# Kernel optimization log

Hardware: AMD Instinct MI355X
Metric: run time of the kernel (lower is better)

The kernel has to match this reference:

```python
import jax, jax.numpy as jnp
import numpy as np


def setup_inputs() -> dict:
    key = jax.random.key(0)
    k1, k2 = jax.random.split(key)
    B, S, D = 8, 2048, 1024
    head = jax.random.normal(k1, (B, S, D), dtype=jnp.float32)
    tail = jax.random.normal(k2, (B, S, D), dtype=jnp.float32)
    return {"head": head, "tail": tail}


def reference(head, tail):
    # head: [B, Sh, D], tail: [B, St, D]; temperature = 1/sqrt(D)
    D = tail.shape[2]
    temperature = 1.0 / jnp.sqrt(jnp.asarray(D, dtype=tail.dtype))
    # scores: [B, St, Sh] = tail @ head^T, scaled
    scores = jnp.einsum('btd,bhd->bth', tail, head) * temperature
    # softmax over the head axis (last dim)
    weight = jax.nn.softmax(scores, axis=-1)
    # pred_tails: [B, St, D] (requires Sh == St, as in the original matmul)
    pred_tails = jnp.einsum('bth,bhd->btd', weight, tail)
    return pred_tails
```

## Files before the change

### kernel.cpp

```cpp
#include <hip/hip_runtime.h>
#include <stdint.h>

typedef __attribute__((ext_vector_type(4))) float f32x4;
typedef __attribute__((ext_vector_type(4))) unsigned int u32x4;
typedef __attribute__((ext_vector_type(8))) __bf16 bf16x8;

#define NB 8
#define SQ 2048
#define DM 1024

__device__ __forceinline__ bf16x8 ldfrag(const __bf16* base, int row, int chunk) {
  const char* p = (const char*)base + row * 128 + ((chunk ^ (row & 7)) << 4);
  return *(const bf16x8*)p;
}

__global__ void k_convert(const float* __restrict__ src, __bf16* __restrict__ dst) {
  size_t i = (size_t)blockIdx.x * blockDim.x + threadIdx.x;
  const f32x4* s = (const f32x4*)src + i * 2;
  f32x4 a = s[0], b = s[1];
  bf16x8 o;
  o[0] = (__bf16)a[0]; o[1] = (__bf16)a[1]; o[2] = (__bf16)a[2]; o[3] = (__bf16)a[3];
  o[4] = (__bf16)b[0]; o[5] = (__bf16)b[1]; o[6] = (__bf16)b[2]; o[7] = (__bf16)b[3];
  *((bf16x8*)dst + i) = o;
}

__global__ void k_transpose(const float* __restrict__ V, __bf16* __restrict__ Vt) {
  __shared__ alignas(16) __bf16 sT[64 * 72];
  const int tid = threadIdx.x;
  const int d0 = blockIdx.x * 64, h0 = blockIdx.y * 64, b = blockIdx.z;
#pragma unroll
  for (int p = 0; p < 4; ++p) {
    int r = (tid >> 4) + p * 16;
    int c4 = (tid & 15) * 4;
    f32x4 v = *(const f32x4*)&V[((size_t)(b * SQ + h0 + r)) * DM + d0 + c4];
#pragma unroll
    for (int j = 0; j < 4; ++j) sT[(c4 + j) * 72 + r] = (__bf16)v[j];
  }
  __syncthreads();
#pragma unroll
  for (int p = 0; p < 2; ++p) {
    int d = (tid >> 3) + p * 32;
    int hc = (tid & 7) * 8;
    u32x4 val = *(const u32x4*)&sT[d * 72 + hc];
    *(u32x4*)&Vt[((size_t)(b * DM + d0 + d)) * SQ + h0 + hc] = val;
  }
}

__launch_bounds__(512)
__global__ void k_scores(const __bf16* __restrict__ Tb, const __bf16* __restrict__ Hb,
                         __bf16* __restrict__ E, float* __restrict__ invl) {
  __shared__ alignas(16) __bf16 sA[2][64 * 64];
  __shared__ alignas(16) __bf16 sB[2][256 * 64];
  __shared__ float s_rs4[4][64];
  const int tid = threadIdx.x;
  const int b = blockIdx.y;
  const int t0 = blockIdx.x * 64;
  const int w = tid >> 6, lane = tid & 63;
  const int wm = w >> 2, wn = w & 3;
  const int lr = lane & 15, lg = lane >> 4;

  const int sr = tid >> 3;
  const int sc = tid & 7;
  const __bf16* Abase = Tb + ((size_t)(b * SQ + t0 + sr)) * DM + ((sc ^ (sr & 7)) * 8);
  const size_t brow = (size_t)64 * DM;

  float rs[2][4];
#pragma unroll
  for (int m = 0; m < 2; ++m)
#pragma unroll
    for (int i = 0; i < 4; ++i) rs[m][i] = 0.f;

  for (int nt = 0; nt < 8; ++nt) {
    const int h0 = nt * 256;
    const __bf16* Bbase = Hb + ((size_t)(b * SQ + h0 + sr)) * DM + ((sc ^ (sr & 7)) * 8);

    f32x4 acc[2][4];
#pragma unroll
    for (int m = 0; m < 2; ++m)
#pragma unroll
      for (int n = 0; n < 4; ++n) acc[m][n] = (f32x4){0.f, 0.f, 0.f, 0.f};

    {
      u32x4 ra = *(const u32x4*)(Abase);
      u32x4 rb[4];
#pragma unroll
      for (int rep = 0; rep < 4; ++rep) rb[rep] = *(const u32x4*)(Bbase + rep * brow);
      *(u32x4*)&sA[0][sr * 64 + sc * 8] = ra;
#pragma unroll
      for (int rep = 0; rep < 4; ++rep)
        *(u32x4*)&sB[0][(sr + rep * 64) * 64 + sc * 8] = rb[rep];
    }
    __syncthreads();

    int cur = 0;
    for (int kt = 0; kt < 16; ++kt) {
      u32x4 na, nb[4];
      const bool more = (kt + 1 < 16);
      if (more) {
        na = *(const u32x4*)(Abase + (kt + 1) * 64);
#pragma unroll
        for (int rep = 0; rep < 4; ++rep)
          nb[rep] = *(const u32x4*)(Bbase + rep * brow + (kt + 1) * 64);
      }
      const __bf16* A = sA[cur];
      const __bf16* Bt = sB[cur];
#pragma unroll
      for (int ks = 0; ks < 2; ++ks) {
        bf16x8 af[2], bfr[4];
#pragma unroll
        for (int m = 0; m < 2; ++m) af[m] = ldfrag(A, wm * 32 + m * 16 + lr, ks * 4 + lg);
#pragma unroll
        for (int n = 0; n < 4; ++n) bfr[n] = ldfrag(Bt, wn * 64 + n * 16 + lr, ks * 4 + lg);
#pragma unroll
        for (int m = 0; m < 2; ++m)
#pragma unroll
          for (int n = 0; n < 4; ++n)
            acc[m][n] = __builtin_amdgcn_mfma_f32_16x16x32_bf16(af[m], bfr[n], acc[m][n], 0, 0, 0);
      }
      if (more) {
        *(u32x4*)&sA[cur ^ 1][sr * 64 + sc * 8] = na;
#pragma unroll
        for (int rep = 0; rep < 4; ++rep)
          *(u32x4*)&sB[cur ^ 1][(sr + rep * 64) * 64 + sc * 8] = nb[rep];
      }
      __syncthreads();
      cur ^= 1;
    }

#pragma unroll
    for (int m = 0; m < 2; ++m)
#pragma unroll
      for (int n = 0; n < 4; ++n)
#pragma unroll
        for (int i = 0; i < 4; ++i) {
          float e = __expf(acc[m][n][i] * 0.03125f);
          int rowl = wm * 32 + m * 16 + lg * 4 + i;
          int col = h0 + wn * 64 + n * 16 + lr;
          E[((size_t)(b * SQ + t0 + rowl)) * SQ + col] = (__bf16)e;
          rs[m][i] += e;
        }
  }

#pragma unroll
  for (int m = 0; m < 2; ++m)
#pragma unroll
    for (int i = 0; i < 4; ++i) {
      float v = rs[m][i];
#pragma unroll
      for (int off = 1; off < 16; off <<= 1) v += __shfl_xor(v, off);
      if (lr == 0) s_rs4[wn][wm * 32 + m * 16 + lg * 4 + i] = v;
    }
  __syncthreads();
  if (tid < 64) {
    float s = s_rs4[0][tid] + s_rs4[1][tid] + s_rs4[2][tid] + s_rs4[3][tid];
    invl[b * SQ + t0 + tid] = 1.0f / s;
  }
}

__launch_bounds__(512)
__global__ void k_pv(const __bf16* __restrict__ E, const __bf16* __restrict__ Vt,
                     const float* __restrict__ invl, float* __restrict__ out) {
  __shared__ alignas(16) __bf16 sA[2][128 * 64];
  __shared__ alignas(16) __bf16 sB[2][128 * 64];
  __shared__ float s_inv[128];
  const int tid = threadIdx.x;
  const int b = blockIdx.z;
  const int t0 = blockIdx.x * 128, d0 = blockIdx.y * 128;
  const int w = tid >> 6, lane = tid & 63;
  const int wm = w >> 1, wn = w & 1;
  const int lr = lane & 15, lg = lane >> 4;
  if (tid < 128) s_inv[tid] = invl[b * SQ + t0 + tid];

  const int sr = tid >> 3, sc = tid & 7;
  const __bf16* Abase = E + ((size_t)(b * SQ + t0 + sr)) * SQ + ((sc ^ (sr & 7)) * 8);
  const __bf16* Bbase = Vt + ((size_t)(b * DM + d0 + sr)) * SQ + ((sc ^ (sr & 7)) * 8);
  const size_t rrow = (size_t)64 * SQ;

  f32x4 acc[2][4];
#pragma unroll
  for (int m = 0; m < 2; ++m)
#pragma unroll
    for (int n = 0; n < 4; ++n) acc[m][n] = (f32x4){0.f, 0.f, 0.f, 0.f};

  {
    u32x4 ra[2], rb[2];
#pragma unroll
    for (int rep = 0; rep < 2; ++rep) {
      ra[rep] = *(const u32x4*)(Abase + rep * rrow);
      rb[rep] = *(const u32x4*)(Bbase + rep * rrow);
    }
#pragma unroll
    for (int rep = 0; rep < 2; ++rep) {
      *(u32x4*)&sA[0][(sr + rep * 64) * 64 + sc * 8] = ra[rep];
      *(u32x4*)&sB[0][(sr + rep * 64) * 64 + sc * 8] = rb[rep];
    }
  }
  __syncthreads();

  int cur = 0;
  for (int kt = 0; kt < 32; ++kt) {
    u32x4 na[2], nb[2];
    const bool more = (kt + 1 < 32);
    if (more) {
#pragma unroll
      for (int rep = 0; rep < 2; ++rep) {
        na[rep] = *(const u32x4*)(Abase + rep * rrow + (kt + 1) * 64);
        nb[rep] = *(const u32x4*)(Bbase + rep * rrow + (kt + 1) * 64);
      }
    }
    const __bf16* A = sA[cur];
    const __bf16* Bt = sB[cur];
#pragma unroll
    for (int ks = 0; ks < 2; ++ks) {
      bf16x8 af[2], bfr[4];
#pragma unroll
      for (int m = 0; m < 2; ++m) af[m] = ldfrag(A, wm * 32 + m * 16 + lr, ks * 4 + lg);
#pragma unroll
      for (int n = 0; n < 4; ++n) bfr[n] = ldfrag(Bt, wn * 64 + n * 16 + lr, ks * 4 + lg);
#pragma unroll
      for (int m = 0; m < 2; ++m)
#pragma unroll
        for (int n = 0; n < 4; ++n)
          acc[m][n] = __builtin_amdgcn_mfma_f32_16x16x32_bf16(af[m], bfr[n], acc[m][n], 0, 0, 0);
    }
    if (more) {
#pragma unroll
      for (int rep = 0; rep < 2; ++rep) {
        *(u32x4*)&sA[cur ^ 1][(sr + rep * 64) * 64 + sc * 8] = na[rep];
        *(u32x4*)&sB[cur ^ 1][(sr + rep * 64) * 64 + sc * 8] = nb[rep];
      }
    }
    __syncthreads();
    cur ^= 1;
  }

#pragma unroll
  for (int m = 0; m < 2; ++m)
#pragma unroll
    for (int n = 0; n < 4; ++n)
#pragma unroll
      for (int i = 0; i < 4; ++i) {
        int rowl = wm * 32 + m * 16 + lg * 4 + i;
        int col = wn * 64 + n * 16 + lr;
        out[((size_t)(b * SQ + t0 + rowl)) * DM + d0 + col] = acc[m][n][i] * s_inv[rowl];
      }
}

extern "C" void kernel_launch(void* const* d_in, const int* in_sizes, int n_in,
                              void* d_out, int out_size, void* d_ws, size_t ws_size,
                              hipStream_t stream) {
  const float* head = (const float*)d_in[0];
  const float* tail = (const float*)d_in[1];
  float* out = (float*)d_out;
  char* ws = (char*)d_ws;

  const size_t SZ_BF = (size_t)NB * SQ * DM * 2;
  __bf16* Tb = (__bf16*)(ws);
  __bf16* Hb = (__bf16*)(ws + SZ_BF);
  __bf16* Vt = (__bf16*)(ws + 2 * SZ_BF);
  __bf16* E  = (__bf16*)(ws + 3 * SZ_BF);
  float*  invl = (float*)(ws + 3 * SZ_BF + (size_t)NB * SQ * SQ * 2);

  const int nconv = (NB * SQ * DM) / 8 / 256;
  k_convert<<<nconv, 256, 0, stream>>>(tail, Tb);
  k_convert<<<nconv, 256, 0, stream>>>(head, Hb);
  k_transpose<<<dim3(DM / 64, SQ / 64, NB), 256, 0, stream>>>(tail, Vt);
  k_scores<<<dim3(SQ / 64, NB), 512, 0, stream>>>(Tb, Hb, E, invl);
  k_pv<<<dim3(SQ / 128, DM / 128, NB), 512, 0, stream>>>(E, Vt, invl, out);
}
```

Baseline: 377.9 us.

## Share a triple-buffered direct-to-LDS GEMM core with larger tiles and fused tail prep

Replaces both GEMM kernels with a shared 256x128-tile core that loads global memory straight into LDS with global_load_lds, keeps three buffers, and interleaves MFMA with explicit waitcnt, barriers and setprio. The scores kernel now splits the key axis across blocks and accumulates row sums with atomicAdd into a zeroed buffer. Block indices are swizzled for cache locality, and the tail conversion and transpose are fused so tail is read once. This aims to raise MFMA use and reduce staging overhead, at the cost of atomics, an extra memset, and occupancy limited to one block per CU.

```diff
diff --git a/kernel.cpp b/kernel.cpp
--- a/kernel.cpp
+++ b/kernel.cpp
@@ -4,14 +4,115 @@
 typedef __attribute__((ext_vector_type(4))) float f32x4;
 typedef __attribute__((ext_vector_type(4))) unsigned int u32x4;
 typedef __attribute__((ext_vector_type(8))) __bf16 bf16x8;
+typedef __attribute__((ext_vector_type(4))) __bf16 bf16x4;
 
 #define NB 8
 #define SQ 2048
 #define DM 1024
 
+__device__ __forceinline__ void gload16(const void* g, void* l) {
+  __builtin_amdgcn_global_load_lds(
+      (const __attribute__((address_space(1))) void*)g,
+      (__attribute__((address_space(3))) void*)l, 16, 0, 0);
+}
+
+__device__ __forceinline__ void memfence_bar() {
+  asm volatile("" ::: "memory");
+  __builtin_amdgcn_s_barrier();
+  asm volatile("" ::: "memory");
+}
+
 __device__ __forceinline__ bf16x8 ldfrag(const __bf16* base, int row, int chunk) {
   const char* p = (const char*)base + row * 128 + ((chunk ^ (row & 7)) << 4);
   return *(const bf16x8*)p;
+}
+
+#define SLOTA (256 * 64)
+#define SLOTB (128 * 64)
+
+template <int NT>
+__device__ __forceinline__ void gemm_core(const char* aBase, size_t ldaB,
+                                          const char* bBase, size_t ldbB,
+                                          __bf16* sA, __bf16* sB,
+                                          f32x4 (&acc)[4][4]) {
+  const int tid = threadIdx.x;
+  const int w = tid >> 6, lane = tid & 63;
+  const int wm = w >> 1, wn = w & 1;
+  const int lr = lane & 15, lg = lane >> 4;
+
+  const char* srcA[4];
+  const char* srcB[2];
+  int dstA[4], dstB[2];
+#pragma unroll
+  for (int i = 0; i < 4; ++i) {
+    int p = i * 512 + tid, r = p >> 3, c = (p & 7) ^ (r & 7);
+    srcA[i] = aBase + (size_t)r * ldaB + c * 16;
+    dstA[i] = p * 8;
+  }
+#pragma unroll
+  for (int i = 0; i < 2; ++i) {
+    int p = i * 512 + tid, r = p >> 3, c = (p & 7) ^ (r & 7);
+    srcB[i] = bBase + (size_t)r * ldbB + c * 16;
+    dstB[i] = p * 8;
+  }
+
+  auto stageA = [&](int t, int i) {
+    gload16(srcA[i] + (size_t)t * 128, sA + (t % 3) * SLOTA + dstA[i]);
+  };
+  auto stageB = [&](int t, int i) {
+    gload16(srcB[i] + (size_t)t * 128, sB + (t % 3) * SLOTB + dstB[i]);
+  };
+
+#pragma unroll
+  for (int t = 0; t < 2; ++t) {
+    stageA(t, 0); stageA(t, 1); stageA(t, 2); stageA(t, 3);
+    stageB(t, 0); stageB(t, 1);
+  }
+  asm volatile("s_waitcnt vmcnt(6)" ::: "memory");
+  memfence_bar();
+
+  for (int t = 0; t < NT; ++t) {
+    const __bf16* A = sA + (t % 3) * SLOTA;
+    const __bf16* B = sB + (t % 3) * SLOTB;
+    const bool st = (t + 2) < NT;
+
+    bf16x8 af[4], bfv[4];
+#pragma unroll
+    for (int m = 0; m < 4; ++m) af[m] = ldfrag(A, wm * 64 + m * 16 + lr, lg);
+#pragma unroll
+    for (int n = 0; n < 4; ++n) bfv[n] = ldfrag(B, wn * 64 + n * 16 + lr, lg);
+    if (st) { stageA(t + 2, 0); stageA(t + 2, 1); stageA(t + 2, 2); }
+    memfence_bar();
+    asm volatile("s_waitcnt lgkmcnt(0)" ::: "memory");
+    __builtin_amdgcn_sched_barrier(0);
+    __builtin_amdgcn_s_setprio(1);
+#pragma unroll
+    for (int m = 0; m < 4; ++m)
+#pragma unroll
+      for (int n = 0; n < 4; ++n)
+        acc[m][n] = __builtin_amdgcn_mfma_f32_16x16x32_bf16(af[m], bfv[n], acc[m][n], 0, 0, 0);
+    __builtin_amdgcn_s_setprio(0);
+    memfence_bar();
+
+#pragma unroll
+    for (int m = 0; m < 4; ++m) af[m] = ldfrag(A, wm * 64 + m * 16 + lr, 4 + lg);
+#pragma unroll
+    for (int n = 0; n < 4; ++n) bfv[n] = ldfrag(B, wn * 64 + n * 16 + lr, 4 + lg);
+    if (st) { stageA(t + 2, 3); stageB(t + 2, 0); stageB(t + 2, 1); }
+    if (t < NT - 2) asm volatile("s_waitcnt vmcnt(6)" ::: "memory");
+    else            asm volatile("s_waitcnt vmcnt(0)" ::: "memory");
+    memfence_bar();
+    asm volatile("s_waitcnt lgkmcnt(0)" ::: "memory");
+    __builtin_amdgcn_sched_barrier(0);
+    __builtin_amdgcn_s_setprio(1);
+#pragma unroll
+    for (int m = 0; m < 4; ++m)
+#pragma unroll
+      for (int n = 0; n < 4; ++n)
+        acc[m][n] = __builtin_amdgcn_mfma_f32_16x16x32_bf16(af[m], bfv[n], acc[m][n], 0, 0, 0);
+    __builtin_amdgcn_s_setprio(0);
+    memfence_bar();
+  }
 }
 
 __global__ void k_convert(const float* __restrict__ src, __bf16* __restrict__ dst) {
@@ -24,7 +125,8 @@
   *((bf16x8*)dst + i) = o;
 }
 
-__global__ void k_transpose(const float* __restrict__ V, __bf16* __restrict__ Vt) {
+__global__ void k_prep_tail(const float* __restrict__ V, __bf16* __restrict__ Tb,
+                            __bf16* __restrict__ Vt) {
   __shared__ alignas(16) __bf16 sT[64 * 72];
   const int tid = threadIdx.x;
   const int d0 = blockIdx.x * 64, h0 = blockIdx.y * 64, b = blockIdx.z;
@@ -33,8 +135,12 @@
     int r = (tid >> 4) + p * 16;
     int c4 = (tid & 15) * 4;
     f32x4 v = *(const f32x4*)&V[((size_t)(b * SQ + h0 + r)) * DM + d0 + c4];
-#pragma unroll
-    for (int j = 0; j < 4; ++j) sT[(c4 + j) * 72 + r] = (__bf16)v[j];
+    bf16x4 o;
+#pragma unroll
+    for (int j = 0; j < 4; ++j) o[j] = (__bf16)v[j];
+    *(bf16x4*)&Tb[((size_t)(b * SQ + h0 + r)) * DM + d0 + c4] = o;
+#pragma unroll
+    for (int j = 0; j < 4; ++j) sT[(c4 + j) * 72 + r] = o[j];
   }
   __syncthreads();
 #pragma unroll
@@ -46,203 +152,93 @@
   }
 }
 
-__launch_bounds__(512)
+__launch_bounds__(512, 1)
 __global__ void k_scores(const __bf16* __restrict__ Tb, const __bf16* __restrict__ Hb,
-                         __bf16* __restrict__ E, float* __restrict__ invl) {
-  __shared__ alignas(16) __bf16 sA[2][64 * 64];
-  __shared__ alignas(16) __bf16 sB[2][256 * 64];
-  __shared__ float s_rs4[4][64];
-  const int tid = threadIdx.x;
-  const int b = blockIdx.y;
-  const int t0 = blockIdx.x * 64;
-  const int w = tid >> 6, lane = tid & 63;
-  const int wm = w >> 2, wn = w & 3;
-  const int lr = lane & 15, lg = lane >> 4;
-
-  const int sr = tid >> 3;
-  const int sc = tid & 7;
-  const __bf16* Abase = Tb + ((size_t)(b * SQ + t0 + sr)) * DM + ((sc ^ (sr & 7)) * 8);
-  const size_t brow = (size_t)64 * DM;
-
-  float rs[2][4];
-#pragma unroll
-  for (int m = 0; m < 2; ++m)
-#pragma unroll
-    for (int i = 0; i < 4; ++i) rs[m][i] = 0.f;
-
-  for (int nt = 0; nt < 8; ++nt) {
-    const int h0 = nt * 256;
-    const __bf16* Bbase = Hb + ((size_t)(b * SQ + h0 + sr)) * DM + ((sc ^ (sr & 7)) * 8);
-
-    f32x4 acc[2][4];
-#pragma unroll
-    for (int m = 0; m < 2; ++m)
-#pragma unroll
-      for (int n = 0; n < 4; ++n) acc[m][n] = (f32x4){0.f, 0.f, 0.f, 0.f};
-
-    {
-      u32x4 ra = *(const u32x4*)(Abase);
-      u32x4 rb[4];
-#pragma unroll
-      for (int rep = 0; rep < 4; ++rep) rb[rep] = *(const u32x4*)(Bbase + rep * brow);
-      *(u32x4*)&sA[0][sr * 64 + sc * 8] = ra;
-#pragma unroll
-      for (int rep = 0; rep < 4; ++rep)
-        *(u32x4*)&sB[0][(sr + rep * 64) * 64 + sc * 8] = rb[rep];
-    }
-    __syncthreads();
-
-    int cur = 0;
-    for (int kt = 0; kt < 16; ++kt) {
-      u32x4 na, nb[4];
-      const bool more = (kt + 1 < 16);
-      if (more) {
-        na = *(const u32x4*)(Abase + (kt + 1) * 64);
-#pragma unroll
-        for (int rep = 0; rep < 4; ++rep)
-          nb[rep] = *(const u32x4*)(Bbase + rep * brow + (kt + 1) * 64);
-      }
-      const __bf16* A = sA[cur];
-      const __bf16* Bt = sB[cur];
-#pragma unroll
-      for (int ks = 0; ks < 2; ++ks) {
-        bf16x8 af[2], bfr[4];
-#pragma unroll
-        for (int m = 0; m < 2; ++m) af[m] = ldfrag(A, wm * 32 + m * 16 + lr, ks * 4 + lg);
-#pragma unroll
-        for (int n = 0; n < 4; ++n) bfr[n] = ldfrag(Bt, wn * 64 + n * 16 + lr, ks * 4 + lg);
-#pragma unroll
-        for (int m = 0; m < 2; ++m)
-#pragma unroll
-          for (int n = 0; n < 4; ++n)
-            acc[m][n] = __builtin_amdgcn_mfma_f32_16x16x32_bf16(af[m], bfr[n], acc[m][n], 0, 0, 0);
-      }
-      if (more) {
-        *(u32x4*)&sA[cur ^ 1][sr * 64 + sc * 8] = na;
-#pragma unroll
-        for (int rep = 0; rep < 4; ++rep)
-          *(u32x4*)&sB[cur ^ 1][(sr + rep * 64) * 64 + sc * 8] = nb[rep];
-      }
-      __syncthreads();
-      cur ^= 1;
-    }
-
-#pragma unroll
-    for (int m = 0; m < 2; ++m)
-#pragma unroll
-      for (int n = 0; n < 4; ++n)
-#pragma unroll
-        for (int i = 0; i < 4; ++i) {
-          float e = __expf(acc[m][n][i] * 0.03125f);
-          int rowl = wm * 32 + m * 16 + lg * 4 + i;
-          int col = h0 + wn * 64 + n * 16 + lr;
-          E[((size_t)(b * SQ + t0 + rowl)) * SQ + col] = (__bf16)e;
-          rs[m][i] += e;
-        }
-  }
-
-#pragma unroll
-  for (int m = 0; m < 2; ++m)
-#pragma unroll
-    for (int i = 0; i < 4; ++i) {
-      float v = rs[m][i];
-#pragma unroll
-      for (int off = 1; off < 16; off <<= 1) v += __shfl_xor(v, off);
-      if (lr == 0) s_rs4[wn][wm * 32 + m * 16 + lg * 4 + i] = v;
-    }
-  __syncthreads();
-  if (tid < 64) {
-    float s = s_rs4[0][tid] + s_rs4[1][tid] + s_rs4[2][tid] + s_rs4[3][tid];
-    invl[b * SQ + t0 + tid] = 1.0f / s;
-  }
-}
-
-__launch_bounds__(512)
-__global__ void k_pv(const __bf16* __restrict__ E, const __bf16* __restrict__ Vt,
-                     const float* __restrict__ invl, float* __restrict__ out) {
-  __shared__ alignas(16) __bf16 sA[2][128 * 64];
-  __shared__ alignas(16) __bf16 sB[2][128 * 64];
-  __shared__ float s_inv[128];
-  const int tid = threadIdx.x;
-  const int b = blockIdx.z;
-  const int t0 = blockIdx.x * 128, d0 = blockIdx.y * 128;
+                         __bf16* __restrict__ E, float* __restrict__ lsum) {
+  __shared__ alignas(16) __bf16 sA[3 * SLOTA];
+  __shared__ alignas(16) __bf16 sB[3 * SLOTB];
+  const int bid = blockIdx.x;
+  const int swz = (bid & 7) * 128 + (bid >> 3);
+  const int b = swz >> 7, rem = swz & 127;
+  const int mt = rem >> 4, nt = rem & 15;
+  const int t0 = mt * 256, n0 = nt * 128;
+  const int tid = threadIdx.x;
   const int w = tid >> 6, lane = tid & 63;
   const int wm = w >> 1, wn = w & 1;
   const int lr = lane & 15, lg = lane >> 4;
-  if (tid < 128) s_inv[tid] = invl[b * SQ + t0 + tid];
-
-  const int sr = tid >> 3, sc = tid & 7;
-  const __bf16* Abase = E + ((size_t)(b * SQ + t0 + sr)) * SQ + ((sc ^ (sr & 7)) * 8);
-  const __bf16* Bbase = Vt + ((size_t)(b * DM + d0 + sr)) * SQ + ((sc ^ (sr & 7)) * 8);
-  const size_t rrow = (size_t)64 * SQ;
-
-  f32x4 acc[2][4];
-#pragma unroll
-  for (int m = 0; m < 2; ++m)
+
+  f32x4 acc[4][4];
+#pragma unroll
+  for (int m = 0; m < 4; ++m)
 #pragma unroll
     for (int n = 0; n < 4; ++n) acc[m][n] = (f32x4){0.f, 0.f, 0.f, 0.f};
 
-  {
-    u32x4 ra[2], rb[2];
-#pragma unroll
-    for (int rep = 0; rep < 2; ++rep) {
-      ra[rep] = *(const u32x4*)(Abase + rep * rrow);
-      rb[rep] = *(const u32x4*)(Bbase + rep * rrow);
+  gemm_core<16>((const char*)(Tb + (size_t)(b * SQ + t0) * DM), (size_t)DM * 2,
+                (const char*)(Hb + (size_t)(b * SQ + n0) * DM), (size_t)DM * 2,
+                sA, sB, acc);
+
+#pragma unroll
+  for (int m = 0; m < 4; ++m) {
+    float rsum[4] = {0.f, 0.f, 0.f, 0.f};
+#pragma unroll
+    for (int n = 0; n < 4; ++n)
+#pragma unroll
+      for (int i = 0; i < 4; ++i) {
+        float e = __expf(acc[m][n][i] * 0.03125f);
+        int rowl = wm * 64 + m * 16 + lg * 4 + i;
+        int col = n0 + wn * 64 + n * 16 + lr;
+        E[((size_t)(b * SQ + t0 + rowl)) * SQ + col] = (__bf16)e;
+        rsum[i] += e;
+      }
+#pragma unroll
+    for (int i = 0; i < 4; ++i) {
+      float v = rsum[i];
+      v += __shfl_xor(v, 1); v += __shfl_xor(v, 2);
+      v += __shfl_xor(v, 4); v += __shfl_xor(v, 8);
+      if (lr == 0)
+        atomicAdd(&lsum[b * SQ + t0 + wm * 64 + m * 16 + lg * 4 + i], v);
     }
-#pragma unroll
-    for (int rep = 0; rep < 2; ++rep) {
-      *(u32x4*)&sA[0][(sr + rep * 64) * 64 + sc * 8] = ra[rep];
-      *(u32x4*)&sB[0][(sr + rep * 64) * 64 + sc * 8] = rb[rep];
-    }
-  }
-  __syncthreads();
-
-  int cur = 0;
-  for (int kt = 0; kt < 32; ++kt) {
-    u32x4 na[2], nb[2];
-    const bool more = (kt + 1 < 32);
-    if (more) {
-#pragma unroll
-      for (int rep = 0; rep < 2; ++rep) {
-        na[rep] = *(const u32x4*)(Abase + rep * rrow + (kt + 1) * 64);
-        nb[rep] = *(const u32x4*)(Bbase + rep * rrow + (kt + 1) * 64);
-      }
-    }
-    const __bf16* A = sA[cur];
-    const __bf16* Bt = sB[cur];
-#pragma unroll
-    for (int ks = 0; ks < 2; ++ks) {
-      bf16x8 af[2], bfr[4];
-#pragma unroll
-      for (int m = 0; m < 2; ++m) af[m] = ldfrag(A, wm * 32 + m * 16 + lr, ks * 4 + lg);
-#pragma unroll
-      for (int n = 0; n < 4; ++n) bfr[n] = ldfrag(Bt, wn * 64 + n * 16 + lr, ks * 4 + lg);
-#pragma unroll
-      for (int m = 0; m < 2; ++m)
-#pragma unroll
-        for (int n = 0; n < 4; ++n)
-          acc[m][n] = __builtin_amdgcn_mfma_f32_16x16x32_bf16(af[m], bfr[n], acc[m][n], 0, 0, 0);
-    }
-    if (more) {
-#pragma unroll
-      for (int rep = 0; rep < 2; ++rep) {
-        *(u32x4*)&sA[cur ^ 1][(sr + rep * 64) * 64 + sc * 8] = na[rep];
-        *(u32x4*)&sB[cur ^ 1][(sr + rep * 64) * 64 + sc * 8] = nb[rep];
-      }
-    }
-    __syncthreads();
-    cur ^= 1;
-  }
-
-#pragma unroll
-  for (int m = 0; m < 2; ++m)
+  }
+}
+
+__launch_bounds__(512, 1)
+__global__ void k_pv(const __bf16* __restrict__ E, const __bf16* __restrict__ Vt,
+                     const float* __restrict__ lsum, float* __restrict__ out) {
+  __shared__ alignas(16) __bf16 sA[3 * SLOTA];
+  __shared__ alignas(16) __bf16 sB[3 * SLOTB];
+  __shared__ float s_inv[256];
+  const int bid = blockIdx.x;
+  const int swz = (bid & 7) * 64 + (bid >> 3);
+  const int b = swz >> 6, rem = swz & 63;
+  const int mt = rem >> 3, dt = rem & 7;
+  const int t0 = mt * 256, d0 = dt * 128;
+  const int tid = threadIdx.x;
+  const int w = tid >> 6, lane = tid & 63;
+  const int wm = w >> 1, wn = w & 1;
+  const int lr = lane & 15, lg = lane >> 4;
+
+  if (tid < 256) s_inv[tid] = 1.0f / lsum[b * SQ + t0 + tid];
+
+  f32x4 acc[4][4];
+#pragma unroll
+  for (int m = 0; m < 4; ++m)
+#pragma unroll
+    for (int n = 0; n < 4; ++n) acc[m][n] = (f32x4){0.f, 0.f, 0.f, 0.f};
+
+  gemm_core<32>((const char*)(E + (size_t)(b * SQ + t0) * SQ), (size_t)SQ * 2,
+                (const char*)(Vt + (size_t)(b * DM + d0) * SQ), (size_t)SQ * 2,
+                sA, sB, acc);
+
+#pragma unroll
+  for (int m = 0; m < 4; ++m)
 #pragma unroll
     for (int n = 0; n < 4; ++n)
 #pragma unroll
       for (int i = 0; i < 4; ++i) {
-        int rowl = wm * 32 + m * 16 + lg * 4 + i;
+        int rowl = wm * 64 + m * 16 + lg * 4 + i;
         int col = wn * 64 + n * 16 + lr;
-        out[((size_t)(b * SQ + t0 + rowl)) * DM + d0 + col] = acc[m][n][i] * s_inv[rowl];
+        out[((size_t)(b * SQ + t0 + rowl)) * DM + d0 + col] =
+            acc[m][n][i] * s_inv[rowl];
       }
 }
 
@@ -258,13 +254,14 @@
   __bf16* Tb = (__bf16*)(ws);
   __bf16* Hb = (__bf16*)(ws + SZ_BF);
   __bf16* Vt = (__bf16*)(ws + 2 * SZ_BF);
-  __bf16* E  = (__bf16*)(ws + 3 * SZ_BF);
-  float*  invl = (float*)(ws + 3 * SZ_BF + (size_t)NB * SQ * SQ * 2);
+  __bf16* E = (__bf16*)(ws + 3 * SZ_BF);
+  float* lsum = (float*)(ws + 3 * SZ_BF + (size_t)NB * SQ * SQ * 2);
+
+  hipMemsetAsync(lsum, 0, (size_t)NB * SQ * 4, stream);
 
   const int nconv = (NB * SQ * DM) / 8 / 256;
-  k_convert<<<nconv, 256, 0, stream>>>(tail, Tb);
   k_convert<<<nconv, 256, 0, stream>>>(head, Hb);
-  k_transpose<<<dim3(DM / 64, SQ / 64, NB), 256, 0, stream>>>(tail, Vt);
-  k_scores<<<dim3(SQ / 64, NB), 512, 0, stream>>>(Tb, Hb, E, invl);
-  k_pv<<<dim3(SQ / 128, DM / 128, NB), 512, 0, stream>>>(E, Vt, invl, out);
-}
+  k_prep_tail<<<dim3(DM / 64, SQ / 64, NB), 256, 0, stream>>>(tail, Tb, Vt);
+  k_scores<<<1024, 512, 0, stream>>>(Tb, Hb, E, lsum);
+  k_pv<<<512, 512, 0, stream>>>(E, Vt, lsum, out);
+}
```

After: 339.7 us. 1.11x faster.
